# Optimization experiments

Hardware: AMD Instinct MI355X
Metric: run time of the kernel (lower is better)

The kernel has to match this reference:

```python
import jax, jax.numpy as jnp
import numpy as np
from jax import lax

NUM_LAYERS = 3
NUM_QUBITS = 8
BATCH = 131072
DIM = 2 ** NUM_QUBITS  # 256


def _rot_mats(params):
    # params: (L, Q, 3) angles for RX, RY, RZ. Returns combined U = RZ @ RY @ RX, (L, Q, 2, 2) complex64.
    half = params * 0.5
    cx = jnp.cos(half[..., 0]).astype(jnp.complex64)
    sx = jnp.sin(half[..., 0]).astype(jnp.complex64)
    cy = jnp.cos(half[..., 1]).astype(jnp.complex64)
    sy = jnp.sin(half[..., 1]).astype(jnp.complex64)
    ezm = jnp.exp(-1j * half[..., 2]).astype(jnp.complex64)
    ezp = jnp.exp(1j * half[..., 2]).astype(jnp.complex64)
    zero = jnp.zeros_like(cx)
    RX = jnp.stack([jnp.stack([cx, -1j * sx], -1), jnp.stack([-1j * sx, cx], -1)], -2)
    RY = jnp.stack([jnp.stack([cy, -sy], -1), jnp.stack([sy, cy], -1)], -2)
    RZ = jnp.stack([jnp.stack([ezm, zero], -1), jnp.stack([zero, ezp], -1)], -2)
    return jnp.einsum('lqij,lqjk,lqkm->lqim', RZ, RY, RX)


def _apply_1q(state, U, wire):
    # state: (B, 2,2,...,2); wire w lives on axis w+1 (PennyLane wire 0 = most significant bit)
    ax = wire + 1
    return jnp.moveaxis(jnp.tensordot(U, state, axes=((1,), (ax,))), 0, ax)


def _apply_cnot(state, ctrl, tgt):
    c_ax, t_ax = ctrl + 1, tgt + 1
    s0 = lax.index_in_dim(state, 0, axis=c_ax, keepdims=True)
    s1 = lax.index_in_dim(state, 1, axis=c_ax, keepdims=True)
    s1 = jnp.flip(s1, axis=t_ax)
    return jnp.concatenate([s0, s1], axis=c_ax)


def _circuit(params, state_re, state_im):
    U = _rot_mats(params)  # (L, Q, 2, 2)
    state = (state_re + 1j * state_im).astype(jnp.complex64)
    state = state.reshape((state.shape[0],) + (2,) * NUM_QUBITS)
    for l in range(NUM_LAYERS):
        for q in range(NUM_QUBITS):
            state = _apply_1q(state, U[l, q], q)
        for q in range(NUM_QUBITS):
            state = _apply_cnot(state, q, (q + 1) % NUM_QUBITS)
    state = state.reshape(state.shape[0], DIM)
    # probability that wire 0 measures |0>: sum |amp|^2 over first half of amplitudes
    half = state[:, : DIM // 2]
    return jnp.sum(half.real ** 2 + half.imag ** 2, axis=1).astype(jnp.float32)


def setup_inputs() -> dict:
    key = jax.random.key(0)
    k1, k2, k3 = jax.random.split(key, 3)
    params = jax.random.uniform(k1, (NUM_LAYERS, NUM_QUBITS, 3), dtype=jnp.float32)
    sr = jax.random.normal(k2, (BATCH, DIM), dtype=jnp.float32)
    si = jax.random.normal(k3, (BATCH, DIM), dtype=jnp.float32)
    norm = jnp.sqrt(jnp.sum(sr ** 2 + si ** 2, axis=1, keepdims=True))
    return {"params": params, "state_re": sr / norm, "state_im": si / norm}


def reference(params, state_re, state_im):
    return _circuit(params, state_re, state_im)
```

## Files before the change

kernel.cpp:

```cpp
#include <hip/hip_runtime.h>
#include <stdint.h>

#define NLAYERS 3
#define NQ 8
#define DIM 256
#define BATCH 131072

typedef float  f32x4  __attribute__((ext_vector_type(4)));
typedef __bf16 bf16x8 __attribute__((ext_vector_type(8)));

__device__ __forceinline__ unsigned short f2bf(float f){
    union { float f; uint32_t u; } v; v.f = f;
    uint32_t u = v.u;
    u += 0x7fffu + ((u >> 16) & 1u);
    return (unsigned short)(u >> 16);
}

__device__ __forceinline__ float2 cmul(float2 a, float2 b){
    return make_float2(a.x*b.x - a.y*b.y, a.x*b.y + a.y*b.x);
}

__device__ __forceinline__ void gload_lds16(void* lds, const void* g){
    __builtin_amdgcn_global_load_lds(
        (const __attribute__((address_space(1))) unsigned int*)g,
        (__attribute__((address_space(3))) unsigned int*)lds,
        16, 0, 0);
}

__global__ __launch_bounds__(256) void build_w_kernel(const float* __restrict__ params,
                                                      unsigned short* __restrict__ W){
    __shared__ float2 st[2][DIM];
    __shared__ float2 gm[NLAYERS*NQ][4];
    const int j = blockIdx.x;
    const int i = threadIdx.x;

    if (i < NLAYERS*NQ){
        const float* pp = params + i*3;
        float hx = 0.5f*pp[0], hy = 0.5f*pp[1], hz = 0.5f*pp[2];
        float cx = cosf(hx), sx = sinf(hx);
        float cy = cosf(hy), sy = sinf(hy);
        float cz = cosf(hz), sz = sinf(hz);
        float2 ezm = make_float2(cz, -sz), ezp = make_float2(cz, sz);
        float2 m00 = make_float2( cy*cx,  sy*sx);
        float2 m01 = make_float2(-sy*cx, -cy*sx);
        float2 m10 = make_float2( sy*cx, -cy*sx);
        float2 m11 = make_float2( cy*cx, -sy*sx);
        gm[i][0] = cmul(ezm, m00);
        gm[i][1] = cmul(ezm, m01);
        gm[i][2] = cmul(ezp, m10);
        gm[i][3] = cmul(ezp, m11);
    }

    int psrc = i;
    #pragma unroll
    for (int q = NQ-1; q >= 0; --q){
        int c  = 7 - q;
        int tb = 7 - ((q + 1) & 7);
        psrc = ((psrc >> c) & 1) ? (psrc ^ (1 << tb)) : psrc;
    }

    int cur = 0;
    st[0][i] = make_float2(i == j ? 1.0f : 0.0f, 0.0f);
    __syncthreads();

    for (int l = 0; l < NLAYERS; ++l){
        for (int q = 0; q < NQ; ++q){
            float2 U0a = gm[l*NQ+q][0], U0b = gm[l*NQ+q][1];
            float2 U1a = gm[l*NQ+q][2], U1b = gm[l*NQ+q][3];
            int p  = 7 - q;
            int bs = (i >> p) & 1;
            int i0 = i & ~(1 << p), i1 = i | (1 << p);
            float2 a0 = st[cur][i0], a1 = st[cur][i1];
            float2 ua = bs ? U1a : U0a;
            float2 ub = bs ? U1b : U0b;
            float2 r;
            r.x = ua.x*a0.x - ua.y*a0.y + ub.x*a1.x - ub.y*a1.y;
            r.y = ua.x*a0.y + ua.y*a0.x + ub.x*a1.y + ub.y*a1.x;
            st[cur ^ 1][i] = r;
            cur ^= 1;
            __syncthreads();
        }
        float2 r = st[cur][psrc];
        st[cur ^ 1][i] = r;
        cur ^= 1;
        __syncthreads();
    }

    const int m = i & 127;
    float2 a = st[cur][m];
    if (i < 128) W[(uint32_t)m*256u + (uint32_t)j]          = f2bf(a.x);
    else         W[32768u + (uint32_t)m*256u + (uint32_t)j] = f2bf(a.y);
}


#define STAGE(B) { \
    gload_lds16(&Abuf[B][(r0+0)*DIM], srcp0); srcp0 += 16*DIM; \
    gload_lds16(&Abuf[B][(r0+1)*DIM], srcp1); srcp1 += 16*DIM; \
    gload_lds16(&Abuf[B][(r0+2)*DIM], srcp2); srcp2 += 16*DIM; \
    gload_lds16(&Abuf[B][(r0+3)*DIM], srcp3); srcp3 += 16*DIM; }

#define BSTEP(S) { \
    f32x4 ra0 = *(const f32x4*)(arow + S*32 + o0); \
    f32x4 ra1 = *(const f32x4*)(arow + S*32 + o1); \
    f32x4 qa0 = *(const f32x4*)(irow + S*32 + o0); \
    f32x4 qa1 = *(const f32x4*)(irow + S*32 + o1); \
    union { f32x4 v; uint32_t u[4]; } ha_, hb_; \
    union { uint32_t u[4]; bf16x8 f; } pr_, pi_, pn_; \
    ha_.v = ra0; hb_.v = ra1; \
    pr_.u[0] = __builtin_amdgcn_perm(ha_.u[1], ha_.u[0], 0x07060302); \
    pr_.u[1] = __builtin_amdgcn_perm(ha_.u[3], ha_.u[2], 0x07060302); \
    pr_.u[2] = __builtin_amdgcn_perm(hb_.u[1], hb_.u[0], 0x07060302); \
    pr_.u[3] = __builtin_amdgcn_perm(hb_.u[3], hb_.u[2], 0x07060302); \
    ha_.v = qa0; hb_.v = qa1; \
    pi_.u[0] = __builtin_amdgcn_perm(ha_.u[1], ha_.u[0], 0x07060302); \
    pi_.u[1] = __builtin_amdgcn_perm(ha_.u[3], ha_.u[2], 0x07060302); \
    pi_.u[2] = __builtin_amdgcn_perm(hb_.u[1], hb_.u[0], 0x07060302); \
    pi_.u[3] = __builtin_amdgcn_perm(hb_.u[3], hb_.u[2], 0x07060302); \
    pn_.u[0] = pi_.u[0] ^ 0x80008000u; \
    pn_.u[1] = pi_.u[1] ^ 0x80008000u; \
    pn_.u[2] = pi_.u[2] ^ 0x80008000u; \
    pn_.u[3] = pi_.u[3] ^ 0x80008000u; \
    accR = __builtin_amdgcn_mfma_f32_16x16x32_bf16(pr_.f, bre_##S, accR, 0, 0, 0); \
    accR = __builtin_amdgcn_mfma_f32_16x16x32_bf16(pn_.f, bim_##S, accR, 0, 0, 0); \
    accI = __builtin_amdgcn_mfma_f32_16x16x32_bf16(pr_.f, bim_##S, accI, 0, 0, 0); \
    accI = __builtin_amdgcn_mfma_f32_16x16x32_bf16(pi_.f, bre_##S, accI, 0, 0, 0); \
}

__global__ __launch_bounds__(512, 4) void qform3_kernel(const float* __restrict__ sr,
                                                        const float* __restrict__ si,
                                                        const unsigned short* __restrict__ W,
                                                        float* __restrict__ out){
    __shared__ float Abuf[2][32*DIM];
    __shared__ float red[128];

    const int tid  = threadIdx.x;
    const int lane = tid & 63;
    const int w    = tid >> 6;
    const int l15  = lane & 15;
    const int quad = lane >> 4;
    const int x7   = l15 & 7;
    const size_t m0 = (size_t)blockIdx.x * 256;

    const int r0 = w * 4;
    const float* plane = (w < 4) ? sr : si;
    const float* srcp0 = plane + (m0 + ((r0+0)&15))*DIM + ((lane ^ ((r0+0)&7)) << 2);
    const float* srcp1 = plane + (m0 + ((r0+1)&15))*DIM + ((lane ^ ((r0+1)&7)) << 2);
    const float* srcp2 = plane + (m0 + ((r0+2)&15))*DIM + ((lane ^ ((r0+2)&7)) << 2);
    const float* srcp3 = plane + (m0 + ((r0+3)&15))*DIM + ((lane ^ ((r0+3)&7)) << 2);

    STAGE(0)

    const unsigned short* wre = W + ((uint32_t)(w*16 + l15))*256u + (uint32_t)(quad*8);
    const unsigned short* wim = wre + 32768u;
    const bf16x8 bre_0 = *(const bf16x8*)(wre + 0*32);
    const bf16x8 bre_1 = *(const bf16x8*)(wre + 1*32);
    const bf16x8 bre_2 = *(const bf16x8*)(wre + 2*32);
    const bf16x8 bre_3 = *(const bf16x8*)(wre + 3*32);
    const bf16x8 bre_4 = *(const bf16x8*)(wre + 4*32);
    const bf16x8 bre_5 = *(const bf16x8*)(wre + 5*32);
    const bf16x8 bre_6 = *(const bf16x8*)(wre + 6*32);
    const bf16x8 bre_7 = *(const bf16x8*)(wre + 7*32);
    const bf16x8 bim_0 = *(const bf16x8*)(wim + 0*32);
    const bf16x8 bim_1 = *(const bf16x8*)(wim + 1*32);
    const bf16x8 bim_2 = *(const bf16x8*)(wim + 2*32);
    const bf16x8 bim_3 = *(const bf16x8*)(wim + 3*32);
    const bf16x8 bim_4 = *(const bf16x8*)(wim + 4*32);
    const bf16x8 bim_5 = *(const bf16x8*)(wim + 5*32);
    const bf16x8 bim_6 = *(const bf16x8*)(wim + 6*32);
    const bf16x8 bim_7 = *(const bf16x8*)(wim + 7*32);

    const int o0 = (((quad << 1)    ) ^ x7) << 2;
    const int o1 = (((quad << 1) | 1) ^ x7) << 2;

    int buf = 0;
    #pragma unroll 1
    for (int t = 0; t < 16; ++t){
        if (t < 15){
            STAGE(buf ^ 1)
            asm volatile("s_waitcnt vmcnt(4)" ::: "memory");
        } else {
            asm volatile("s_waitcnt vmcnt(0)" ::: "memory");
        }
        __builtin_amdgcn_s_barrier();
        __builtin_amdgcn_sched_barrier(0);

        const float* arow = &Abuf[buf][l15 * DIM];
        const float* irow = &Abuf[buf][(16 + l15) * DIM];

        f32x4 accR = {0.0f, 0.0f, 0.0f, 0.0f};
        f32x4 accI = {0.0f, 0.0f, 0.0f, 0.0f};
        BSTEP(0) BSTEP(1) BSTEP(2) BSTEP(3)
        BSTEP(4) BSTEP(5) BSTEP(6) BSTEP(7)

        #pragma unroll
        for (int r = 0; r < 4; ++r){
            const float vr = accR[r], vi = accI[r];
            float tt = vr*vr + vi*vi;
            tt += __shfl_xor(tt, 1);
            tt += __shfl_xor(tt, 2);
            tt += __shfl_xor(tt, 4);
            tt += __shfl_xor(tt, 8);
            if (l15 == 0) red[w*16 + quad*4 + r] = tt;
        }
        asm volatile("s_waitcnt lgkmcnt(0)" ::: "memory");
        __builtin_amdgcn_s_barrier();
        __builtin_amdgcn_sched_barrier(0);

        if (tid < 16){
            float o = 0.0f;
            #pragma unroll
            for (int ww = 0; ww < 8; ++ww) o += red[ww*16 + tid];
            out[m0 + t*16 + tid] = o;
        }
        buf ^= 1;
    }
}

extern "C" void kernel_launch(void* const* d_in, const int* in_sizes, int n_in,
                              void* d_out, int out_size, void* d_ws, size_t ws_size,
                              hipStream_t stream){
    const float* params = (const float*)d_in[0];
    const float* sr     = (const float*)d_in[1];
    const float* si     = (const float*)d_in[2];
    unsigned short* Wimg = (unsigned short*)d_ws;
    float* out          = (float*)d_out;

    build_w_kernel<<<dim3(DIM), dim3(256), 0, stream>>>(params, Wimg);
    qform3_kernel<<<dim3(512), dim3(512), 0, stream>>>(sr, si, Wimg, out);
}
```

Before: 294.7 us.

## Halve block size so each wave covers two W column tiles

Blocks shrink from 8 waves to 4, and each wave now holds two 16-column slices of the W matrix in registers. Each A fragment loaded from LDS is reused for two sets of MFMAs, which halves the LDS reads and bf16 conversion work per MFMA. The grid doubles to 1024 blocks of 128 rows each with 8 row tiles per block, and each wave issues twice as many global-to-LDS loads per stage. The cost is higher VGPR pressure from 32 resident B fragments and fewer waves to hide memory latency.

```diff
diff --git a/kernel.cpp b/kernel.cpp
--- a/kernel.cpp
+++ b/kernel.cpp
@@ -94,10 +94,18 @@
 
 
 #define STAGE(B) { \
-    gload_lds16(&Abuf[B][(r0+0)*DIM], srcp0); srcp0 += 16*DIM; \
-    gload_lds16(&Abuf[B][(r0+1)*DIM], srcp1); srcp1 += 16*DIM; \
-    gload_lds16(&Abuf[B][(r0+2)*DIM], srcp2); srcp2 += 16*DIM; \
-    gload_lds16(&Abuf[B][(r0+3)*DIM], srcp3); srcp3 += 16*DIM; }
+    gload_lds16(&Abuf[B][(c0+0)*DIM], srcp0); srcp0 += 16*DIM; \
+    gload_lds16(&Abuf[B][(c0+1)*DIM], srcp1); srcp1 += 16*DIM; \
+    gload_lds16(&Abuf[B][(c0+2)*DIM], srcp2); srcp2 += 16*DIM; \
+    gload_lds16(&Abuf[B][(c0+3)*DIM], srcp3); srcp3 += 16*DIM; \
+    gload_lds16(&Abuf[B][(c0+4)*DIM], srcp4); srcp4 += 16*DIM; \
+    gload_lds16(&Abuf[B][(c0+5)*DIM], srcp5); srcp5 += 16*DIM; \
+    gload_lds16(&Abuf[B][(c0+6)*DIM], srcp6); srcp6 += 16*DIM; \
+    gload_lds16(&Abuf[B][(c0+7)*DIM], srcp7); srcp7 += 16*DIM; }
+
+#define LOADB(F, S) \
+    const bf16x8 bre_##F##_##S = *(const bf16x8*)(wrp##F + S*32); \
+    const bf16x8 bim_##F##_##S = *(const bf16x8*)(wrp##F + 32768 + S*32);
 
 #define BSTEP(S) { \
     f32x4 ra0 = *(const f32x4*)(arow + S*32 + o0); \
@@ -120,18 +128,23 @@
     pn_.u[1] = pi_.u[1] ^ 0x80008000u; \
     pn_.u[2] = pi_.u[2] ^ 0x80008000u; \
     pn_.u[3] = pi_.u[3] ^ 0x80008000u; \
-    accR = __builtin_amdgcn_mfma_f32_16x16x32_bf16(pr_.f, bre_##S, accR, 0, 0, 0); \
-    accR = __builtin_amdgcn_mfma_f32_16x16x32_bf16(pn_.f, bim_##S, accR, 0, 0, 0); \
-    accI = __builtin_amdgcn_mfma_f32_16x16x32_bf16(pr_.f, bim_##S, accI, 0, 0, 0); \
-    accI = __builtin_amdgcn_mfma_f32_16x16x32_bf16(pi_.f, bre_##S, accI, 0, 0, 0); \
-}
-
-__global__ __launch_bounds__(512, 4) void qform3_kernel(const float* __restrict__ sr,
+    const bf16x8 fr_ = pr_.f, fi_ = pi_.f, fn_ = pn_.f; \
+    accR0 = __builtin_amdgcn_mfma_f32_16x16x32_bf16(fr_, bre_0_##S, accR0, 0, 0, 0); \
+    accR0 = __builtin_amdgcn_mfma_f32_16x16x32_bf16(fn_, bim_0_##S, accR0, 0, 0, 0); \
+    accI0 = __builtin_amdgcn_mfma_f32_16x16x32_bf16(fr_, bim_0_##S, accI0, 0, 0, 0); \
+    accI0 = __builtin_amdgcn_mfma_f32_16x16x32_bf16(fi_, bre_0_##S, accI0, 0, 0, 0); \
+    accR1 = __builtin_amdgcn_mfma_f32_16x16x32_bf16(fr_, bre_1_##S, accR1, 0, 0, 0); \
+    accR1 = __builtin_amdgcn_mfma_f32_16x16x32_bf16(fn_, bim_1_##S, accR1, 0, 0, 0); \
+    accI1 = __builtin_amdgcn_mfma_f32_16x16x32_bf16(fr_, bim_1_##S, accI1, 0, 0, 0); \
+    accI1 = __builtin_amdgcn_mfma_f32_16x16x32_bf16(fi_, bre_1_##S, accI1, 0, 0, 0); \
+}
+
+__global__ __launch_bounds__(256, 2) void qform4_kernel(const float* __restrict__ sr,
                                                         const float* __restrict__ si,
                                                         const unsigned short* __restrict__ W,
                                                         float* __restrict__ out){
     __shared__ float Abuf[2][32*DIM];
-    __shared__ float red[128];
+    __shared__ float red[64];
 
     const int tid  = threadIdx.x;
     const int lane = tid & 63;
@@ -139,45 +152,38 @@
     const int l15  = lane & 15;
     const int quad = lane >> 4;
     const int x7   = l15 & 7;
-    const size_t m0 = (size_t)blockIdx.x * 256;
-
-    const int r0 = w * 4;
-    const float* plane = (w < 4) ? sr : si;
-    const float* srcp0 = plane + (m0 + ((r0+0)&15))*DIM + ((lane ^ ((r0+0)&7)) << 2);
-    const float* srcp1 = plane + (m0 + ((r0+1)&15))*DIM + ((lane ^ ((r0+1)&7)) << 2);
-    const float* srcp2 = plane + (m0 + ((r0+2)&15))*DIM + ((lane ^ ((r0+2)&7)) << 2);
-    const float* srcp3 = plane + (m0 + ((r0+3)&15))*DIM + ((lane ^ ((r0+3)&7)) << 2);
+    const size_t m0 = (size_t)blockIdx.x * 128;
+
+    const int c0 = w * 8;
+    #define SRCP(I) ((((c0+I) < 16) ? sr : si) + (m0 + ((c0+I)&15))*DIM + ((lane ^ ((c0+I)&7)) << 2))
+    const float* srcp0 = SRCP(0);
+    const float* srcp1 = SRCP(1);
+    const float* srcp2 = SRCP(2);
+    const float* srcp3 = SRCP(3);
+    const float* srcp4 = SRCP(4);
+    const float* srcp5 = SRCP(5);
+    const float* srcp6 = SRCP(6);
+    const float* srcp7 = SRCP(7);
+    #undef SRCP
 
     STAGE(0)
 
-    const unsigned short* wre = W + ((uint32_t)(w*16 + l15))*256u + (uint32_t)(quad*8);
-    const unsigned short* wim = wre + 32768u;
-    const bf16x8 bre_0 = *(const bf16x8*)(wre + 0*32);
-    const bf16x8 bre_1 = *(const bf16x8*)(wre + 1*32);
-    const bf16x8 bre_2 = *(const bf16x8*)(wre + 2*32);
-    const bf16x8 bre_3 = *(const bf16x8*)(wre + 3*32);
-    const bf16x8 bre_4 = *(const bf16x8*)(wre + 4*32);
-    const bf16x8 bre_5 = *(const bf16x8*)(wre + 5*32);
-    const bf16x8 bre_6 = *(const bf16x8*)(wre + 6*32);
-    const bf16x8 bre_7 = *(const bf16x8*)(wre + 7*32);
-    const bf16x8 bim_0 = *(const bf16x8*)(wim + 0*32);
-    const bf16x8 bim_1 = *(const bf16x8*)(wim + 1*32);
-    const bf16x8 bim_2 = *(const bf16x8*)(wim + 2*32);
-    const bf16x8 bim_3 = *(const bf16x8*)(wim + 3*32);
-    const bf16x8 bim_4 = *(const bf16x8*)(wim + 4*32);
-    const bf16x8 bim_5 = *(const bf16x8*)(wim + 5*32);
-    const bf16x8 bim_6 = *(const bf16x8*)(wim + 6*32);
-    const bf16x8 bim_7 = *(const bf16x8*)(wim + 7*32);
+    const unsigned short* wrp0 = W + ((uint32_t)(w*32 +  0 + l15))*256u + (uint32_t)(quad*8);
+    const unsigned short* wrp1 = W + ((uint32_t)(w*32 + 16 + l15))*256u + (uint32_t)(quad*8);
+    LOADB(0,0) LOADB(0,1) LOADB(0,2) LOADB(0,3)
+    LOADB(0,4) LOADB(0,5) LOADB(0,6) LOADB(0,7)
+    LOADB(1,0) LOADB(1,1) LOADB(1,2) LOADB(1,3)
+    LOADB(1,4) LOADB(1,5) LOADB(1,6) LOADB(1,7)
 
     const int o0 = (((quad << 1)    ) ^ x7) << 2;
     const int o1 = (((quad << 1) | 1) ^ x7) << 2;
 
     int buf = 0;
     #pragma unroll 1
-    for (int t = 0; t < 16; ++t){
-        if (t < 15){
+    for (int t = 0; t < 8; ++t){
+        if (t < 7){
             STAGE(buf ^ 1)
-            asm volatile("s_waitcnt vmcnt(4)" ::: "memory");
+            asm volatile("s_waitcnt vmcnt(8)" ::: "memory");
         } else {
             asm volatile("s_waitcnt vmcnt(0)" ::: "memory");
         }
@@ -187,15 +193,16 @@
         const float* arow = &Abuf[buf][l15 * DIM];
         const float* irow = &Abuf[buf][(16 + l15) * DIM];
 
-        f32x4 accR = {0.0f, 0.0f, 0.0f, 0.0f};
-        f32x4 accI = {0.0f, 0.0f, 0.0f, 0.0f};
+        f32x4 accR0 = {0.f,0.f,0.f,0.f}, accI0 = {0.f,0.f,0.f,0.f};
+        f32x4 accR1 = {0.f,0.f,0.f,0.f}, accI1 = {0.f,0.f,0.f,0.f};
         BSTEP(0) BSTEP(1) BSTEP(2) BSTEP(3)
         BSTEP(4) BSTEP(5) BSTEP(6) BSTEP(7)
 
         #pragma unroll
         for (int r = 0; r < 4; ++r){
-            const float vr = accR[r], vi = accI[r];
-            float tt = vr*vr + vi*vi;
+            const float v0 = accR0[r], u0 = accI0[r];
+            const float v1 = accR1[r], u1 = accI1[r];
+            float tt = v0*v0 + u0*u0 + v1*v1 + u1*u1;
             tt += __shfl_xor(tt, 1);
             tt += __shfl_xor(tt, 2);
             tt += __shfl_xor(tt, 4);
@@ -207,10 +214,7 @@
         __builtin_amdgcn_sched_barrier(0);
 
         if (tid < 16){
-            float o = 0.0f;
-            #pragma unroll
-            for (int ww = 0; ww < 8; ++ww) o += red[ww*16 + tid];
-            out[m0 + t*16 + tid] = o;
+            out[m0 + t*16 + tid] = red[tid] + red[16 + tid] + red[32 + tid] + red[48 + tid];
         }
         buf ^= 1;
     }
@@ -226,5 +230,5 @@
     float* out          = (float*)d_out;
 
     build_w_kernel<<<dim3(DIM), dim3(256), 0, stream>>>(params, Wimg);
-    qform3_kernel<<<dim3(512), dim3(512), 0, stream>>>(sr, si, Wimg, out);
-}
+    qform4_kernel<<<dim3(1024), dim3(256), 0, stream>>>(sr, si, Wimg, out);
+}
```

After: 301.8 us. 2.4% more time.
